# Kernel optimization log

Hardware: AMD Instinct MI355X
Metric: run time of the kernel (lower is better)

## Reference

```python
import jax, jax.numpy as jnp
import numpy as np

B, T, S, D, H, FF = 4, 1024, 1024, 1024, 16, 4096
DH = D // H
NEG = -1e9
EPS = 1e-5


def setup_inputs() -> dict:
    key = jax.random.key(0)
    ks = jax.random.split(key, 20)
    p = 0.02  # param init scale
    inp = {
        "x": jax.random.normal(ks[0], (B, T, D), jnp.float32),
        "encoder_output": jax.random.normal(ks[1], (B, S, D), jnp.float32),
        "src_mask": jnp.ones((B, 1, 1, S), jnp.bool_),
        "tgt_mask": jnp.tril(jnp.ones((1, 1, T, T), jnp.bool_)),  # causal
        # self-attention params
        "d_Wq": jax.random.normal(ks[2], (D, D)) * p, "d_bq": jnp.zeros((D,)),
        "d_Wk": jax.random.normal(ks[3], (D, D)) * p, "d_bk": jnp.zeros((D,)),
        "d_Wv": jax.random.normal(ks[4], (D, D)) * p, "d_bv": jnp.zeros((D,)),
        "d_Wo": jax.random.normal(ks[5], (D, D)) * p, "d_bo": jnp.zeros((D,)),
        # cross-attention params
        "e_Wq": jax.random.normal(ks[6], (D, D)) * p, "e_bq": jnp.zeros((D,)),
        "e_Wk": jax.random.normal(ks[7], (D, D)) * p, "e_bk": jnp.zeros((D,)),
        "e_Wv": jax.random.normal(ks[8], (D, D)) * p, "e_bv": jnp.zeros((D,)),
        "e_Wo": jax.random.normal(ks[9], (D, D)) * p, "e_bo": jnp.zeros((D,)),
        # FFN params
        "ff_W1": jax.random.normal(ks[10], (D, FF)) * p, "ff_b1": jnp.zeros((FF,)),
        "ff_W2": jax.random.normal(ks[11], (FF, D)) * p, "ff_b2": jnp.zeros((D,)),
        # layernorm params
        "ln1_g": jnp.ones((D,)), "ln1_b": jnp.zeros((D,)),
        "ln2_g": jnp.ones((D,)), "ln2_b": jnp.zeros((D,)),
        "ln3_g": jnp.ones((D,)), "ln3_b": jnp.zeros((D,)),
    }
    return inp


def _mha(xq, xkv, Wq, bq, Wk, bk, Wv, bv, Wo, bo, mask):
    b, tq = xq.shape[0], xq.shape[1]
    q = (xq @ Wq + bq).reshape(b, tq, H, DH).transpose(0, 2, 1, 3)
    k = (xkv @ Wk + bk).reshape(b, -1, H, DH).transpose(0, 2, 1, 3)
    v = (xkv @ Wv + bv).reshape(b, -1, H, DH).transpose(0, 2, 1, 3)
    scores = jnp.einsum("bhqd,bhkd->bhqk", q, k) / np.float32(np.sqrt(DH))
    scores = jnp.where(mask, scores, NEG)
    attn = jax.nn.softmax(scores, axis=-1)
    out = jnp.einsum("bhqk,bhkd->bhqd", attn, v)
    out = out.transpose(0, 2, 1, 3).reshape(b, tq, D)
    return out @ Wo + bo


def _ln(x, g, b):
    m = jnp.mean(x, axis=-1, keepdims=True)
    v = jnp.var(x, axis=-1, keepdims=True)
    return (x - m) / jnp.sqrt(v + EPS) * g + b


def reference(x, encoder_output, src_mask, tgt_mask,
              d_Wq, d_bq, d_Wk, d_bk, d_Wv, d_bv, d_Wo, d_bo,
              e_Wq, e_bq, e_Wk, e_bk, e_Wv, e_bv, e_Wo, e_bo,
              ff_W1, ff_b1, ff_W2, ff_b2,
              ln1_g, ln1_b, ln2_g, ln2_b, ln3_g, ln3_b):
    # masked self-attention + residual + LN (dropout is identity in eval)
    d = _mha(x, x, d_Wq, d_bq, d_Wk, d_bk, d_Wv, d_bv, d_Wo, d_bo, tgt_mask)
    d = _ln(d + x, ln1_g, ln1_b)
    # cross-attention over encoder output + residual + LN
    f = _mha(d, encoder_output, e_Wq, e_bq, e_Wk, e_bk, e_Wv, e_bv, e_Wo, e_bo, src_mask)
    f = _ln(f + d, ln2_g, ln2_b)
    # FFN + residual + LN
    g = jax.nn.relu(f @ ff_W1 + ff_b1) @ ff_W2 + ff_b2
    g = _ln(g + f, ln3_g, ln3_b)
    return g
```

## Files before the change

kernel.cpp:

```cpp
#include <hip/hip_runtime.h>

static constexpr int Bc = 4, Tc = 1024, Sc = 1024, Dc = 1024, Hc = 16, DHc = 64, FFc = 4096;

typedef __attribute__((ext_vector_type(8))) short short8;
typedef __attribute__((ext_vector_type(4))) short short4v;
typedef __attribute__((ext_vector_type(4))) float f32x4;

__device__ __forceinline__ unsigned short f2bf(float f) {
    unsigned int u = __float_as_uint(f);
    unsigned int r = u + 0x7fffu + ((u >> 16) & 1u);
    return (unsigned short)(r >> 16);
}
__device__ __forceinline__ float bf2f(unsigned short u) {
    return __uint_as_float(((unsigned int)u) << 16);
}

__device__ __forceinline__ void gload_lds16(const void* g, void* l) {
    __builtin_amdgcn_global_load_lds((const __attribute__((address_space(1))) void*)g,
                                     (__attribute__((address_space(3))) void*)l, 16, 0, 0);
}

__global__ __launch_bounds__(256) void cast_f32_bf16(const float* __restrict__ in,
                                                     unsigned short* __restrict__ out, int n8) {
    int i = blockIdx.x * 256 + threadIdx.x;
    if (i >= n8) return;
    const float4* p = (const float4*)in + (size_t)i * 2;
    float4 a = p[0], b = p[1];
    short8 o;
    o[0] = f2bf(a.x); o[1] = f2bf(a.y); o[2] = f2bf(a.z); o[3] = f2bf(a.w);
    o[4] = f2bf(b.x); o[5] = f2bf(b.y); o[6] = f2bf(b.z); o[7] = f2bf(b.w);
    *(short8*)(out + (size_t)i * 8) = o;
}

__global__ __launch_bounds__(256) void transpose_cast(const float* __restrict__ W,
                                                      unsigned short* __restrict__ Wt,
                                                      int K, int N) {
    __shared__ float tile[32][33];
    int n0 = blockIdx.x * 32, k0 = blockIdx.y * 32;
    int tx = threadIdx.x, ty = threadIdx.y;
#pragma unroll
    for (int i = 0; i < 4; i++)
        tile[ty + i * 8][tx] = W[(size_t)(k0 + ty + i * 8) * N + n0 + tx];
    __syncthreads();
#pragma unroll
    for (int i = 0; i < 4; i++)
        Wt[(size_t)(n0 + ty + i * 8) * K + k0 + tx] = f2bf(tile[tx][ty + i * 8]);
}

struct TP8 { const float* s[8]; unsigned short* d[8]; };
__global__ __launch_bounds__(256) void transpose_cast8(TP8 p) {
    __shared__ float tile[32][33];
    const float* W = p.s[blockIdx.z];
    unsigned short* Wt = p.d[blockIdx.z];
    int n0 = blockIdx.x * 32, k0 = blockIdx.y * 32;
    int tx = threadIdx.x, ty = threadIdx.y;
#pragma unroll
    for (int i = 0; i < 4; i++)
        tile[ty + i * 8][tx] = W[(size_t)(k0 + ty + i * 8) * 1024 + n0 + tx];
    __syncthreads();
#pragma unroll
    for (int i = 0; i < 4; i++)
        Wt[(size_t)(n0 + ty + i * 8) * 1024 + k0 + tx] = f2bf(tile[tx][ty + i * 8]);
}

__global__ void concat_bias(const float* b0, const float* b1, const float* b2,
                            float* __restrict__ out) {
    int i = blockIdx.x * 256 + threadIdx.x;
    int seg = i >> 10, j = i & 1023;
    const float* p = seg == 0 ? b0 : (seg == 1 ? b1 : b2);
    out[i] = p[j];
}

__global__ __launch_bounds__(256) void transpose_v(const unsigned short* __restrict__ V, int ldv,
                                                   unsigned short* __restrict__ Vt) {
    __shared__ unsigned short t[64 * 64];
    const int bh = blockIdx.y, b = bh >> 4, h = bh & 15;
    const int s0 = blockIdx.x * 64;
    const int tid = threadIdx.x;
    const int r = tid >> 2, ch = tid & 3;
    const unsigned short* src = V + (size_t)(b * 1024 + s0 + r) * ldv + h * 64 + ch * 16;
    short8 v0 = *(const short8*)src;
    short8 v1 = *(const short8*)(src + 8);
    int pw_ = (ch ^ r ^ (r >> 4)) & 3;
    *(short8*)(t + r * 64 + pw_ * 16) = v0;
    *(short8*)(t + r * 64 + pw_ * 16 + 8) = v1;
    __syncthreads();
    const int dh = tid >> 2, sc = (tid & 3) * 16;
    short8 o0, o1;
#pragma unroll
    for (int j = 0; j < 8; j++) {
        int c0 = sc + j, c1 = sc + 8 + j;
        o0[j] = t[c0 * 64 + (((dh >> 4) ^ c0 ^ (c0 >> 4)) & 3) * 16 + (dh & 15)];
        o1[j] = t[c1 * 64 + (((dh >> 4) ^ c1 ^ (c1 >> 4)) & 3) * 16 + (dh & 15)];
    }
    unsigned short* dst = Vt + ((size_t)bh * 64 + dh) * 1024 + s0 + sc;
    *(short8*)dst = o0;
    *(short8*)(dst + 8) = o1;
}

struct BlkMap { int m, n, z; };
__device__ __forceinline__ BlkMap remap_block() {
    const int gx = gridDim.x, gy = gridDim.y;
    const int nxy = gx * gy;
    const int nwg = nxy * gridDim.z;
    const int flat = (blockIdx.z * gy + blockIdx.y) * gx + blockIdx.x;
    const int id = (flat & 7) * (nwg >> 3) + (flat >> 3);
    const int pz = id / nxy;
    const int rz = id - pz * nxy;
    const int gsz = 8 * gy;
    const int grp = rz / gsz;
    const int rem = rz - grp * gsz;
    BlkMap r;
    r.m = rem >> 3;
    r.n = grp * 8 + (rem & 7);
    r.z = pz;
    return r;
}

template <int EPI>
__global__ __launch_bounds__(256) void gemm_db(const unsigned short* __restrict__ A,
                                               const unsigned short* __restrict__ Bt,
                                               const float* __restrict__ bias,
                                               float* __restrict__ outF,
                                               unsigned short* __restrict__ outB,
                                               int M, int N, int Kloop, int lda, int ldb) {
    __shared__ unsigned short As[3][128 * 32];
    __shared__ unsigned short Bs[3][128 * 32];
    const int tid = threadIdx.x;
    const int w = tid >> 6, lane = tid & 63, l4 = lane & 15, g = lane >> 4;
    BlkMap bm = remap_block();
    const int m0 = bm.m * 128, n0 = bm.n * 128, z = bm.z;
    A += (size_t)z * Kloop;
    Bt += (size_t)z * Kloop;
    const int wr = w >> 1, wc = w & 1;
    f32x4 acc[4][4] = {};
    const int r0 = tid >> 2;
    const int kk = ((tid & 3) ^ ((tid >> 3) & 3)) * 8;
    const int sk = (l4 >> 1) & 3;
    const unsigned short* Ar0 = A + (size_t)(m0 + r0) * lda + kk;
    const unsigned short* Ar1 = A + (size_t)(m0 + 64 + r0) * lda + kk;
    const unsigned short* Br0 = Bt + (size_t)(n0 + r0) * ldb + kk;
    const unsigned short* Br1 = Bt + (size_t)(n0 + 64 + r0) * ldb + kk;
    auto stage = [&](int sb, int k0) {
        gload_lds16(Ar0 + k0, (char*)As[sb] + tid * 16);
        gload_lds16(Ar1 + k0, (char*)As[sb] + 4096 + tid * 16);
        gload_lds16(Br0 + k0, (char*)Bs[sb] + tid * 16);
        gload_lds16(Br1 + k0, (char*)Bs[sb] + 4096 + tid * 16);
    };
    const int nk = Kloop >> 5;
    stage(0, 0);
    stage(1, 32);
    asm volatile("s_waitcnt vmcnt(4)" ::: "memory");
    __builtin_amdgcn_s_barrier();
    asm volatile("" ::: "memory");
    int buf = 0;
    for (int t = 0; t < nk; ++t) {
        if (t + 2 < nk) {
            int b2 = buf + 2; if (b2 >= 3) b2 -= 3;
            stage(b2, (t + 2) * 32);
        }
        short8 a[4], b[4];
#pragma unroll
        for (int m = 0; m < 4; m++)
            a[m] = *(const short8*)(As[buf] + (wr * 64 + m * 16 + l4) * 32 + (g ^ sk) * 8);
#pragma unroll
        for (int n = 0; n < 4; n++)
            b[n] = *(const short8*)(Bs[buf] + (wc * 64 + n * 16 + l4) * 32 + (g ^ sk) * 8);
#pragma unroll
        for (int m = 0; m < 4; m++)
#pragma unroll
            for (int n = 0; n < 4; n++)
                acc[m][n] = __builtin_amdgcn_mfma_f32_16x16x32_bf16(a[m], b[n], acc[m][n], 0, 0, 0);
        if (t + 1 < nk) {
            if (t + 2 < nk) asm volatile("s_waitcnt vmcnt(4)" ::: "memory");
            else            asm volatile("s_waitcnt vmcnt(0)" ::: "memory");
            __builtin_amdgcn_s_barrier();
            asm volatile("" ::: "memory");
        }
        buf = (buf + 1 == 3) ? 0 : buf + 1;
    }
    const int rowB = m0 + wr * 64 + g * 4;
    const int colB = n0 + wc * 64 + l4;
    float* oF = (EPI == 1) ? outF + (size_t)z * M * N : outF;
#pragma unroll
    for (int n = 0; n < 4; n++) {
        float bv = (EPI == 1 && z != 0) ? 0.f : bias[colB + n * 16];
#pragma unroll
        for (int m = 0; m < 4; m++) {
#pragma unroll
            for (int r = 0; r < 4; r++) {
                float v = acc[m][n][r] + bv;
                if (EPI == 2) v = fmaxf(v, 0.f);
                size_t idx = (size_t)(rowB + m * 16 + r) * N + colB + n * 16;
                if (EPI == 1) oF[idx] = v;
                else outB[idx] = f2bf(v);
            }
        }
    }
}

template <int EPI>
__global__ __launch_bounds__(256) void gemm64_db(const unsigned short* __restrict__ A,
                                                 const unsigned short* __restrict__ Bt,
                                                 const float* __restrict__ bias,
                                                 float* __restrict__ outF,
                                                 unsigned short* __restrict__ outB,
                                                 int M, int N, int Kloop, int lda, int ldb) {
    __shared__ unsigned short As[3][64 * 32];
    __shared__ unsigned short Bs[3][128 * 32];
    const int tid = threadIdx.x;
    const int w = tid >> 6, lane = tid & 63, l4 = lane & 15, g = lane >> 4;
    BlkMap bm = remap_block();
    const int m0 = bm.m * 64, n0 = bm.n * 128;
    f32x4 acc[4][2] = {};
    const int r0 = tid >> 2;
    const int kk = ((tid & 3) ^ ((tid >> 3) & 3)) * 8;
    const int sk = (l4 >> 1) & 3;
    const unsigned short* Ar0 = A + (size_t)(m0 + r0) * lda + kk;
    const unsigned short* Br0 = Bt + (size_t)(n0 + r0) * ldb + kk;
    const unsigned short* Br1 = Bt + (size_t)(n0 + 64 + r0) * ldb + kk;
    auto stage = [&](int sb, int k0) {
        gload_lds16(Ar0 + k0, (char*)As[sb] + tid * 16);
        gload_lds16(Br0 + k0, (char*)Bs[sb] + tid * 16);
        gload_lds16(Br1 + k0, (char*)Bs[sb] + 4096 + tid * 16);
    };
    const int nk = Kloop >> 5;
    stage(0, 0);
    stage(1, 32);
    asm volatile("s_waitcnt vmcnt(3)" ::: "memory");
    __builtin_amdgcn_s_barrier();
    asm volatile("" ::: "memory");
    int buf = 0;
    for (int t = 0; t < nk; ++t) {
        if (t + 2 < nk) {
            int b2 = buf + 2; if (b2 >= 3) b2 -= 3;
            stage(b2, (t + 2) * 32);
        }
        short8 a[4], b[2];
#pragma unroll
        for (int m = 0; m < 4; m++)
            a[m] = *(const short8*)(As[buf] + (m * 16 + l4) * 32 + (g ^ sk) * 8);
#pragma unroll
        for (int n = 0; n < 2; n++)
            b[n] = *(const short8*)(Bs[buf] + (w * 32 + n * 16 + l4) * 32 + (g ^ sk) * 8);
#pragma unroll
        for (int m = 0; m < 4; m++)
#pragma unroll
            for (int n = 0; n < 2; n++)
                acc[m][n] = __builtin_amdgcn_mfma_f32_16x16x32_bf16(a[m], b[n], acc[m][n], 0, 0, 0);
        if (t + 1 < nk) {
            if (t + 2 < nk) asm volatile("s_waitcnt vmcnt(3)" ::: "memory");
            else            asm volatile("s_waitcnt vmcnt(0)" ::: "memory");
            __builtin_amdgcn_s_barrier();
            asm volatile("" ::: "memory");
        }
        buf = (buf + 1 == 3) ? 0 : buf + 1;
    }
    const int rowB = m0 + g * 4;
    const int colB = n0 + w * 32 + l4;
#pragma unroll
    for (int n = 0; n < 2; n++) {
        float bv = bias[colB + n * 16];
#pragma unroll
        for (int m = 0; m < 4; m++) {
#pragma unroll
            for (int r = 0; r < 4; r++) {
                float v = acc[m][n][r] + bv;
                if (EPI == 2) v = fmaxf(v, 0.f);
                size_t idx = (size_t)(rowB + m * 16 + r) * N + colB + n * 16;
                if (EPI == 1) outF[idx] = v;
                else outB[idx] = f2bf(v);
            }
        }
    }
}

template <int CAUSAL>
__global__ __launch_bounds__(256) void attn4_kernel(const unsigned short* __restrict__ Q, int ldq,
                                                    const unsigned short* __restrict__ Kg, int ldk,
                                                    const unsigned short* __restrict__ Vt,
                                                    unsigned short* __restrict__ O) {
    __shared__ unsigned short Kl[2 * 64 * 64];
    __shared__ unsigned short Vl[2 * 64 * 64];
    __shared__ unsigned short Pl[4][16 * 72];
    const int bh = blockIdx.x, qb = blockIdx.y;
    const int b = bh >> 4, h = bh & 15;
    const int tid = threadIdx.x, w = tid >> 6, lane = tid & 63;
    const int l4 = lane & 15, g = lane >> 4;
    const int q0 = qb * 64 + w * 16;
    const unsigned short* Qp = Q + (size_t)(b * Tc + q0 + l4) * ldq + h * DHc + g * 8;
    short8 qf0 = *(const short8*)Qp;
    short8 qf1 = *(const short8*)(Qp + 32);
    const unsigned short* Kbase = Kg + (size_t)(b * 1024) * ldk + h * DHc;
    const unsigned short* Vbase = Vt + (size_t)bh * DHc * 1024;
    f32x4 o[4] = {};
    float mrun = -1e30f, lrun = 0.f;
    const int nT = CAUSAL ? qb + 1 : 16;
    unsigned short* pw = &Pl[w][l4 * 72];
    const int qi = q0 + l4;

    const int sr0 = tid >> 3;
    const int sr1 = 32 + sr0;
    const int sc_ = (tid & 7) ^ (sr0 & 7);

    auto stage = [&](int s0, int buf) {
        char* kd = (char*)Kl + buf * 8192;
        char* vd = (char*)Vl + buf * 8192;
        gload_lds16(Kbase + (size_t)(s0 + sr0) * ldk + sc_ * 8, kd + tid * 16);
        gload_lds16(Kbase + (size_t)(s0 + sr1) * ldk + sc_ * 8, kd + 4096 + tid * 16);
        gload_lds16(Vbase + (size_t)sr0 * 1024 + s0 + sc_ * 8, vd + tid * 16);
        gload_lds16(Vbase + (size_t)sr1 * 1024 + s0 + sc_ * 8, vd + 4096 + tid * 16);
    };

    stage(0, 0);
    __syncthreads();
    int buf = 0;
    const int sw = l4 & 7;

    for (int t = 0; t < nT; ++t) {
        const int s0 = t * 64;
        if (t + 1 < nT) stage(s0 + 64, buf ^ 1);
        const unsigned short* Kb_ = Kl + buf * 4096;
        const unsigned short* Vb_ = Vl + buf * 4096;
        f32x4 st[4];
        f32x4 z = {0.f, 0.f, 0.f, 0.f};
        __builtin_amdgcn_s_setprio(1);
#pragma unroll
        for (int c = 0; c < 4; c++) {
            const unsigned short* kr = Kb_ + (c * 16 + l4) * 64;
            short8 ka0 = *(const short8*)(kr + ((g ^ sw) * 8));
            short8 ka1 = *(const short8*)(kr + (((g + 4) ^ sw) * 8));
            st[c] = __builtin_amdgcn_mfma_f32_16x16x32_bf16(ka0, qf0, z, 0, 0, 0);
            st[c] = __builtin_amdgcn_mfma_f32_16x16x32_bf16(ka1, qf1, st[c], 0, 0, 0);
        }
        __builtin_amdgcn_s_setprio(0);
        float p[16];
        float tmax = -1e30f;
        const bool domask = CAUSAL && (t == nT - 1);
#pragma unroll
        for (int c = 0; c < 4; c++)
#pragma unroll
            for (int r = 0; r < 4; r++) {
                float v = st[c][r] * 0.125f;
                if (domask && (s0 + c * 16 + g * 4 + r) > qi) v = -1e9f;
                p[c * 4 + r] = v;
                tmax = fmaxf(tmax, v);
            }
        tmax = fmaxf(tmax, __shfl_xor(tmax, 16));
        tmax = fmaxf(tmax, __shfl_xor(tmax, 32));
        if (!__all(tmax <= mrun + 8.f)) {
            float mnew = fmaxf(mrun, tmax);
            float al = __expf(mrun - mnew);
            lrun *= al;
#pragma unroll
            for (int d = 0; d < 4; d++) o[d] *= al;
            mrun = mnew;
        }
        float ps = 0.f;
#pragma unroll
        for (int i = 0; i < 16; i++) { p[i] = __expf(p[i] - mrun); ps += p[i]; }
        ps += __shfl_xor(ps, 16);
        ps += __shfl_xor(ps, 32);
        lrun += ps;
#pragma unroll
        for (int c = 0; c < 4; c++) {
            short4v pk;
            pk[0] = f2bf(p[c * 4 + 0]); pk[1] = f2bf(p[c * 4 + 1]);
            pk[2] = f2bf(p[c * 4 + 2]); pk[3] = f2bf(p[c * 4 + 3]);
            *(short4v*)(pw + c * 16 + g * 4) = pk;
        }
        short8 pb_lo = *(const short8*)(pw + g * 8);
        short8 pb_hi = *(const short8*)(pw + 32 + g * 8);
        __builtin_amdgcn_s_setprio(1);
#pragma unroll
        for (int d = 0; d < 4; d++) {
            const unsigned short* vr = Vb_ + (d * 16 + l4) * 64;
            short8 va0 = *(const short8*)(vr + ((g ^ sw) * 8));
            short8 va1 = *(const short8*)(vr + (((g + 4) ^ sw) * 8));
            o[d] = __builtin_amdgcn_mfma_f32_16x16x32_bf16(va0, pb_lo, o[d], 0, 0, 0);
            o[d] = __builtin_amdgcn_mfma_f32_16x16x32_bf16(va1, pb_hi, o[d], 0, 0, 0);
        }
        __builtin_amdgcn_s_setprio(0);
        __syncthreads();
        buf ^= 1;
    }
    float inv = 1.f / lrun;
    unsigned short* Ob = O + (size_t)(b * Tc + q0 + l4) * Dc + h * DHc;
#pragma unroll
    for (int d = 0; d < 4; d++) {
#pragma unroll
        for (int r = 0; r < 4; r++) Ob[d * 16 + g * 4 + r] = f2bf(o[d][r] * inv);
    }
}

__global__ __launch_bounds__(256) void ln_bf(const unsigned short* __restrict__ a,
                                             const unsigned short* __restrict__ res,
                                             const float* __restrict__ gam,
                                             const float* __restrict__ bet,
                                             unsigned short* __restrict__ outB,
                                             float* __restrict__ outF) {
    int row = blockIdx.x, t = threadIdx.x;
    size_t base = (size_t)row * Dc + t * 4;
    short4v av = *(const short4v*)(a + base);
    short4v rv = *(const short4v*)(res + base);
    float x0 = bf2f((unsigned short)av[0]) + bf2f((unsigned short)rv[0]);
    float x1 = bf2f((unsigned short)av[1]) + bf2f((unsigned short)rv[1]);
    float x2 = bf2f((unsigned short)av[2]) + bf2f((unsigned short)rv[2]);
    float x3 = bf2f((unsigned short)av[3]) + bf2f((unsigned short)rv[3]);
    float s = x0 + x1 + x2 + x3;
    float ss = x0 * x0 + x1 * x1 + x2 * x2 + x3 * x3;
    for (int o = 1; o < 64; o <<= 1) { s += __shfl_xor(s, o); ss += __shfl_xor(ss, o); }
    __shared__ float S1[4], S2[4];
    int w = t >> 6;
    if ((t & 63) == 0) { S1[w] = s; S2[w] = ss; }
    __syncthreads();
    s = S1[0] + S1[1] + S1[2] + S1[3];
    ss = S2[0] + S2[1] + S2[2] + S2[3];
    float mean = s * (1.f / Dc);
    float var = ss * (1.f / Dc) - mean * mean;
    float rstd = rsqrtf(var + 1e-5f);
    int c = t * 4;
    float4 g4 = *(const float4*)(gam + c);
    float4 b4 = *(const float4*)(bet + c);
    float y0 = (x0 - mean) * rstd * g4.x + b4.x;
    float y1 = (x1 - mean) * rstd * g4.y + b4.y;
    float y2 = (x2 - mean) * rstd * g4.z + b4.z;
    float y3 = (x3 - mean) * rstd * g4.w + b4.w;
    if (outB) {
        short4v ob;
        ob[0] = f2bf(y0); ob[1] = f2bf(y1); ob[2] = f2bf(y2); ob[3] = f2bf(y3);
        *(short4v*)(outB + base) = ob;
    }
    if (outF) { float4 ov = {y0, y1, y2, y3}; *(float4*)(outF + base) = ov; }
}

__global__ __launch_bounds__(256) void ln_2f(const float* __restrict__ a0,
                                             const float* __restrict__ a1,
                                             const unsigned short* __restrict__ res,
                                             const float* __restrict__ gam,
                                             const float* __restrict__ bet,
                                             unsigned short* __restrict__ outB,
                                             float* __restrict__ outF) {
    int row = blockIdx.x, t = threadIdx.x;
    size_t base = (size_t)row * Dc + t * 4;
    float4 u = *(const float4*)(a0 + base);
    float4 v = *(const float4*)(a1 + base);
    short4v rv = *(const short4v*)(res + base);
    float x0 = u.x + v.x + bf2f((unsigned short)rv[0]);
    float x1 = u.y + v.y + bf2f((unsigned short)rv[1]);
    float x2 = u.z + v.z + bf2f((unsigned short)rv[2]);
    float x3 = u.w + v.w + bf2f((unsigned short)rv[3]);
    float s = x0 + x1 + x2 + x3;
    float ss = x0 * x0 + x1 * x1 + x2 * x2 + x3 * x3;
    for (int o = 1; o < 64; o <<= 1) { s += __shfl_xor(s, o); ss += __shfl_xor(ss, o); }
    __shared__ float S1[4], S2[4];
    int w = t >> 6;
    if ((t & 63) == 0) { S1[w] = s; S2[w] = ss; }
    __syncthreads();
    s = S1[0] + S1[1] + S1[2] + S1[3];
    ss = S2[0] + S2[1] + S2[2] + S2[3];
    float mean = s * (1.f / Dc);
    float var = ss * (1.f / Dc) - mean * mean;
    float rstd = rsqrtf(var + 1e-5f);
    int c = t * 4;
    float4 g4 = *(const float4*)(gam + c);
    float4 b4 = *(const float4*)(bet + c);
    float y0 = (x0 - mean) * rstd * g4.x + b4.x;
    float y1 = (x1 - mean) * rstd * g4.y + b4.y;
    float y2 = (x2 - mean) * rstd * g4.z + b4.z;
    float y3 = (x3 - mean) * rstd * g4.w + b4.w;
    if (outB) {
        short4v ob;
        ob[0] = f2bf(y0); ob[1] = f2bf(y1); ob[2] = f2bf(y2); ob[3] = f2bf(y3);
        *(short4v*)(outB + base) = ob;
    }
    if (outF) { float4 ov = {y0, y1, y2, y3}; *(float4*)(outF + base) = ov; }
}

extern "C" void kernel_launch(void* const* d_in, const int* in_sizes, int n_in,
                              void* d_out, int out_size, void* d_ws, size_t ws_size,
                              hipStream_t stream) {
    const float* x   = (const float*)d_in[0];
    const float* enc = (const float*)d_in[1];
    const float* dWq = (const float*)d_in[4];  const float* dbq = (const float*)d_in[5];
    const float* dWk = (const float*)d_in[6];  const float* dbk = (const float*)d_in[7];
    const float* dWv = (const float*)d_in[8];  const float* dbv = (const float*)d_in[9];
    const float* dWo = (const float*)d_in[10]; const float* dbo = (const float*)d_in[11];
    const float* eWq = (const float*)d_in[12]; const float* ebq = (const float*)d_in[13];
    const float* eWk = (const float*)d_in[14]; const float* ebk = (const float*)d_in[15];
    const float* eWv = (const float*)d_in[16]; const float* ebv = (const float*)d_in[17];
    const float* eWo = (const float*)d_in[18]; const float* ebo = (const float*)d_in[19];
    const float* fW1 = (const float*)d_in[20]; const float* fb1 = (const float*)d_in[21];
    const float* fW2 = (const float*)d_in[22]; const float* fb2 = (const float*)d_in[23];
    const float* g1 = (const float*)d_in[24];  const float* be1 = (const float*)d_in[25];
    const float* g2 = (const float*)d_in[26];  const float* be2 = (const float*)d_in[27];
    const float* g3 = (const float*)d_in[28];  const float* be3 = (const float*)d_in[29];

    char* ws = (char*)d_ws;
    size_t off = 0;
    auto alloc = [&](size_t bytes) -> void* {
        void* p = ws + off;
        off += (bytes + 255) & ~(size_t)255;
        return p;
    };
    const size_t A = (size_t)4096 * 1024;
    const size_t MB1 = (size_t)1024 * 1024;
    char* R1 = (char*)alloc(32 * 1024 * 1024);
    unsigned short* qkv = (unsigned short*)R1;
    unsigned short* kvx = (unsigned short*)R1;
    unsigned short* qx  = (unsigned short*)(R1 + 16 * 1024 * 1024);
    unsigned short* h1  = (unsigned short*)R1;
    unsigned short* xb   = (unsigned short*)alloc(A * 2);
    unsigned short* encb = (unsigned short*)alloc(A * 2);
    unsigned short* wqkv = (unsigned short*)alloc(3 * MB1 * 2);
    unsigned short* wekv = (unsigned short*)alloc(2 * MB1 * 2);
    unsigned short* weq  = (unsigned short*)alloc(MB1 * 2);
    unsigned short* wdo  = (unsigned short*)alloc(MB1 * 2);
    unsigned short* weo  = (unsigned short*)alloc(MB1 * 2);
    unsigned short* wf1  = (unsigned short*)alloc(4 * MB1 * 2);
    unsigned short* wf2  = (unsigned short*)alloc(4 * MB1 * 2);
    float* bqkv = (float*)alloc(3072 * 4);
    float* bekv = (float*)alloc(2048 * 4);
    unsigned short* VtB = (unsigned short*)alloc(A * 2);
    unsigned short* ab  = (unsigned short*)alloc(A * 2);
    unsigned short* tmpB = (unsigned short*)alloc(A * 2);
    unsigned short* dB = (unsigned short*)alloc(A * 2);
    unsigned short* fB = (unsigned short*)alloc(A * 2);
    float* pf0 = (float*)VtB;
    float* pf1 = pf0 + A;
    (void)ws_size; (void)in_sizes; (void)n_in; (void)out_size;

    dim3 tb(32, 8);
    cast_f32_bf16<<<2048, 256, 0, stream>>>(x, xb, (int)(A / 8));
    cast_f32_bf16<<<2048, 256, 0, stream>>>(enc, encb, (int)(A / 8));
    TP8 tp;
    tp.s[0] = dWq; tp.d[0] = wqkv;
    tp.s[1] = dWk; tp.d[1] = wqkv + MB1;
    tp.s[2] = dWv; tp.d[2] = wqkv + 2 * MB1;
    tp.s[3] = eWk; tp.d[3] = wekv;
    tp.s[4] = eWv; tp.d[4] = wekv + MB1;
    tp.s[5] = eWq; tp.d[5] = weq;
    tp.s[6] = dWo; tp.d[6] = wdo;
    tp.s[7] = eWo; tp.d[7] = weo;
    transpose_cast8<<<dim3(32, 32, 8), tb, 0, stream>>>(tp);
    transpose_cast<<<dim3(128, 32), tb, 0, stream>>>(fW1, wf1, 1024, 4096);
    transpose_cast<<<dim3(32, 128), tb, 0, stream>>>(fW2, wf2, 4096, 1024);
    concat_bias<<<12, 256, 0, stream>>>(dbq, dbk, dbv, bqkv);
    concat_bias<<<8, 256, 0, stream>>>(ebk, ebv, ebv, bekv);

    gemm_db<0><<<dim3(24, 32, 1), 256, 0, stream>>>(xb, wqkv, bqkv, nullptr, qkv, 4096, 3072, 1024, 1024, 1024);
    transpose_v<<<dim3(16, 64), 256, 0, stream>>>(qkv + 2048, 3072, VtB);
    attn4_kernel<1><<<dim3(64, 16), 256, 0, stream>>>(qkv, 3072, qkv + 1024, 3072, VtB, ab);
    gemm64_db<0><<<dim3(8, 64), 256, 0, stream>>>(ab, wdo, dbo, nullptr, tmpB, 4096, 1024, 1024, 1024, 1024);
    ln_bf<<<4096, 256, 0, stream>>>(tmpB, xb, g1, be1, dB, nullptr);

    gemm_db<0><<<dim3(16, 32, 1), 256, 0, stream>>>(encb, wekv, bekv, nullptr, kvx, 4096, 2048, 1024, 1024, 1024);
    gemm64_db<0><<<dim3(8, 64), 256, 0, stream>>>(dB, weq, ebq, nullptr, qx, 4096, 1024, 1024, 1024, 1024);
    transpose_v<<<dim3(16, 64), 256, 0, stream>>>(kvx + 1024, 2048, VtB);
    attn4_kernel<0><<<dim3(64, 16), 256, 0, stream>>>(qx, 1024, kvx, 2048, VtB, ab);
    gemm64_db<0><<<dim3(8, 64), 256, 0, stream>>>(ab, weo, ebo, nullptr, tmpB, 4096, 1024, 1024, 1024, 1024);
    ln_bf<<<4096, 256, 0, stream>>>(tmpB, dB, g2, be2, fB, nullptr);

    gemm_db<2><<<dim3(32, 32, 1), 256, 0, stream>>>(fB, wf1, fb1, nullptr, h1, 4096, 4096, 1024, 1024, 1024);
    gemm_db<1><<<dim3(8, 32, 2), 256, 0, stream>>>(h1, wf2, fb2, pf0, nullptr, 4096, 1024, 2048, 4096, 4096);
    ln_2f<<<4096, 256, 0, stream>>>(pf0, pf1, fB, g3, be3, nullptr, (float*)d_out);
}
```

Baseline: 365.5 us.

## Add 256x256-tile 8-wave GEMM for QKV and FFN1 projections

Adds a new GEMM kernel with 256x256 output tiles, 512 threads, a BK=64 double buffer loaded directly into LDS, and interleaved loads and MFMA phases using setprio. It replaces the 128x128 gemm_db for the fused QKV projection and the FFN up-projection. The goal is higher arithmetic intensity and fewer global/LDS loads per flop. It also changes the block remap to use group width 4 when the grid x is not a multiple of 8. Trade-offs are higher register and LDS pressure, fewer blocks (192 and 256) on the 256-CU part, which risks tail imbalance, and a scalar, uncoalesced bf16 epilogue store.

```diff
diff --git a/kernel.cpp b/kernel.cpp
--- a/kernel.cpp
+++ b/kernel.cpp
@@ -107,14 +107,136 @@
     const int id = (flat & 7) * (nwg >> 3) + (flat >> 3);
     const int pz = id / nxy;
     const int rz = id - pz * nxy;
-    const int gsz = 8 * gy;
+    const int gwsh = (gx & 7) ? 2 : 3;
+    const int gw = 1 << gwsh;
+    const int gsz = gw * gy;
     const int grp = rz / gsz;
     const int rem = rz - grp * gsz;
     BlkMap r;
-    r.m = rem >> 3;
-    r.n = grp * 8 + (rem & 7);
+    r.m = rem >> gwsh;
+    r.n = (grp << gwsh) + (rem & (gw - 1));
     r.z = pz;
     return r;
+}
+
+template <int EPI>
+__global__ __launch_bounds__(512, 2) void gemm256(const unsigned short* __restrict__ A,
+                                                  const unsigned short* __restrict__ Bt,
+                                                  const float* __restrict__ bias,
+                                                  unsigned short* __restrict__ outB,
+                                                  int N, int lda, int ldb, int nk) {
+    __shared__ unsigned short sm[4][16384];
+    const int tid = threadIdx.x;
+    const int lane = tid & 63, wid = tid >> 6;
+    const int l4 = lane & 15, g = lane >> 4;
+    const int wr = wid >> 2, wc = wid & 3;
+    BlkMap bm = remap_block();
+    const int m0 = bm.m * 256, n0 = bm.n * 256;
+    const int srow = tid >> 3;
+    const int schunk = (tid & 7) ^ (srow & 7);
+    const int sw = l4 & 7;
+
+    auto stA = [&](int sb, int seg, int k0) {
+        gload_lds16(A + (size_t)(m0 + seg * 64 + srow) * lda + k0 + schunk * 8,
+                    (char*)sm[sb] + seg * 8192 + tid * 16);
+    };
+    auto stB = [&](int sb, int seg, int k0) {
+        gload_lds16(Bt + (size_t)(n0 + seg * 64 + srow) * ldb + k0 + schunk * 8,
+                    (char*)sm[2 + sb] + seg * 8192 + tid * 16);
+    };
+
+    f32x4 acc[8][4] = {};
+#pragma unroll
+    for (int s = 0; s < 4; s++) stB(0, s, 0);
+#pragma unroll
+    for (int s = 0; s < 4; s++) stA(0, s, 0);
+    asm volatile("s_waitcnt vmcnt(0)" ::: "memory");
+    __builtin_amdgcn_s_barrier();
+
+    for (int t = 0; t < nk; ++t) {
+        const int bufR = t & 1, bufW = bufR ^ 1;
+        const int kn = (t + 1) * 64;
+        const bool pf = (t + 1 < nk);
+        const unsigned short* As_ = sm[bufR];
+        const unsigned short* Bs_ = sm[2 + bufR];
+        short8 a[4], b0[4], b1[4];
+        if (pf) { stB(bufW, 0, kn); stB(bufW, 1, kn); }
+#pragma unroll
+        for (int n = 0; n < 4; n++)
+            b0[n] = *(const short8*)(Bs_ + (wc * 64 + n * 16 + l4) * 64 + (g ^ sw) * 8);
+#pragma unroll
+        for (int m = 0; m < 4; m++)
+            a[m] = *(const short8*)(As_ + (wr * 128 + m * 16 + l4) * 64 + (g ^ sw) * 8);
+        __builtin_amdgcn_s_barrier();
+        __builtin_amdgcn_s_setprio(1);
+#pragma unroll
+        for (int m = 0; m < 4; m++)
+#pragma unroll
+            for (int n = 0; n < 4; n++)
+                acc[m][n] = __builtin_amdgcn_mfma_f32_16x16x32_bf16(a[m], b0[n], acc[m][n], 0, 0, 0);
+        __builtin_amdgcn_s_setprio(0);
+        __builtin_amdgcn_s_barrier();
+        if (pf) { stB(bufW, 2, kn); stB(bufW, 3, kn); }
+#pragma unroll
+        for (int n = 0; n < 4; n++)
+            b1[n] = *(const short8*)(Bs_ + (wc * 64 + n * 16 + l4) * 64 + ((4 + g) ^ sw) * 8);
+#pragma unroll
+        for (int m = 0; m < 4; m++)
+            a[m] = *(const short8*)(As_ + (wr * 128 + m * 16 + l4) * 64 + ((4 + g) ^ sw) * 8);
+        __builtin_amdgcn_s_barrier();
+        __builtin_amdgcn_s_setprio(1);
+#pragma unroll
+        for (int m = 0; m < 4; m++)
+#pragma unroll
+            for (int n = 0; n < 4; n++)
+                acc[m][n] = __builtin_amdgcn_mfma_f32_16x16x32_bf16(a[m], b1[n], acc[m][n], 0, 0, 0);
+        __builtin_amdgcn_s_setprio(0);
+        if (pf) asm volatile("s_waitcnt vmcnt(4)" ::: "memory");
+        else    asm volatile("s_waitcnt vmcnt(0)" ::: "memory");
+        __builtin_amdgcn_s_barrier();
+        if (pf) { stA(bufW, 0, kn); stA(bufW, 2, kn); }
+#pragma unroll
+        for (int m = 0; m < 4; m++)
+            a[m] = *(const short8*)(As_ + (wr * 128 + 64 + m * 16 + l4) * 64 + (g ^ sw) * 8);
+        __builtin_amdgcn_s_barrier();
+        __builtin_amdgcn_s_setprio(1);
+#pragma unroll
+        for (int m = 0; m < 4; m++)
+#pragma unroll
+            for (int n = 0; n < 4; n++)
+                acc[4 + m][n] = __builtin_amdgcn_mfma_f32_16x16x32_bf16(a[m], b0[n], acc[4 + m][n], 0, 0, 0);
+        __builtin_amdgcn_s_setprio(0);
+        __builtin_amdgcn_s_barrier();
+        if (pf) { stA(bufW, 1, kn); stA(bufW, 3, kn); }
+#pragma unroll
+        for (int m = 0; m < 4; m++)
+            a[m] = *(const short8*)(As_ + (wr * 128 + 64 + m * 16 + l4) * 64 + ((4 + g) ^ sw) * 8);
+        __builtin_amdgcn_s_barrier();
+        __builtin_amdgcn_s_setprio(1);
+#pragma unroll
+        for (int m = 0; m < 4; m++)
+#pragma unroll
+            for (int n = 0; n < 4; n++)
+                acc[4 + m][n] = __builtin_amdgcn_mfma_f32_16x16x32_bf16(a[m], b1[n], acc[4 + m][n], 0, 0, 0);
+        __builtin_amdgcn_s_setprio(0);
+        if (pf) asm volatile("s_waitcnt vmcnt(2)" ::: "memory");
+        __builtin_amdgcn_s_barrier();
+    }
+    const int rowB = m0 + wr * 128 + g * 4;
+    const int colB = n0 + wc * 64 + l4;
+#pragma unroll
+    for (int n = 0; n < 4; n++) {
+        float bv = bias[colB + n * 16];
+#pragma unroll
+        for (int m = 0; m < 8; m++) {
+#pragma unroll
+            for (int r = 0; r < 4; r++) {
+                float v = acc[m][n][r] + bv;
+                if (EPI == 2) v = fmaxf(v, 0.f);
+                outB[(size_t)(rowB + m * 16 + r) * N + colB + n * 16] = f2bf(v);
+            }
+        }
+    }
 }
 
 template <int EPI>
@@ -548,7 +670,7 @@
     concat_bias<<<12, 256, 0, stream>>>(dbq, dbk, dbv, bqkv);
     concat_bias<<<8, 256, 0, stream>>>(ebk, ebv, ebv, bekv);
 
-    gemm_db<0><<<dim3(24, 32, 1), 256, 0, stream>>>(xb, wqkv, bqkv, nullptr, qkv, 4096, 3072, 1024, 1024, 1024);
+    gemm256<0><<<dim3(12, 16), 512, 0, stream>>>(xb, wqkv, bqkv, qkv, 3072, 1024, 1024, 16);
     transpose_v<<<dim3(16, 64), 256, 0, stream>>>(qkv + 2048, 3072, VtB);
     attn4_kernel<1><<<dim3(64, 16), 256, 0, stream>>>(qkv, 3072, qkv + 1024, 3072, VtB, ab);
     gemm64_db<0><<<dim3(8, 64), 256, 0, stream>>>(ab, wdo, dbo, nullptr, tmpB, 4096, 1024, 1024, 1024, 1024);
@@ -561,7 +683,7 @@
     gemm64_db<0><<<dim3(8, 64), 256, 0, stream>>>(ab, weo, ebo, nullptr, tmpB, 4096, 1024, 1024, 1024, 1024);
     ln_bf<<<4096, 256, 0, stream>>>(tmpB, dB, g2, be2, fB, nullptr);
 
-    gemm_db<2><<<dim3(32, 32, 1), 256, 0, stream>>>(fB, wf1, fb1, nullptr, h1, 4096, 4096, 1024, 1024, 1024);
+    gemm256<2><<<dim3(16, 16), 512, 0, stream>>>(fB, wf1, fb1, h1, 4096, 1024, 1024, 16);
     gemm_db<1><<<dim3(8, 32, 2), 256, 0, stream>>>(h1, wf2, fb2, pf0, nullptr, 4096, 1024, 2048, 4096, 4096);
     ln_2f<<<4096, 256, 0, stream>>>(pf0, pf1, fB, g3, be3, nullptr, (float*)d_out);
 }
```

Measured after the change: 363.1 us. No clear change (-0.7%).
